# Optimization experiments

Hardware: AMD Instinct MI355X
Metric: run time of the kernel (lower is better)

## Reference

```python
import jax, jax.numpy as jnp
import numpy as np

N_EMBD = 1024
N_HEAD = 16
HEAD_DIM = N_EMBD // N_HEAD


def setup_inputs() -> dict:
    key = jax.random.key(0)
    kx, kq, kk, kv, ko = jax.random.split(key, 5)
    B, T = 4, 2048
    x = jax.random.normal(kx, (B, T, N_EMBD), dtype=jnp.float32)
    s = N_EMBD ** -0.5
    Wq = jax.random.normal(kq, (N_EMBD, N_EMBD), dtype=jnp.float32) * s
    Wk = jax.random.normal(kk, (N_EMBD, HEAD_DIM), dtype=jnp.float32) * s
    Wv = jax.random.normal(kv, (N_EMBD, HEAD_DIM), dtype=jnp.float32) * s
    Wo = jax.random.normal(ko, (N_EMBD, N_EMBD), dtype=jnp.float32) * s
    return {"x": x, "Wq": Wq, "Wk": Wk, "Wv": Wv, "Wo": Wo}


def reference(x, Wq, Wk, Wv, Wo):
    B, T, C = x.shape
    scale = HEAD_DIM ** -0.5
    # q: [B, H, T, D]; shared k, v: [B, T, D]
    q = (x @ Wq).reshape(B, T, N_HEAD, HEAD_DIM).transpose(0, 2, 1, 3)
    k = x @ Wk
    v = x @ Wv
    # scores: [B, H, T, T] (shared K head broadcast over H)
    att = jnp.einsum('bhtd,bsd->bhts', q, k) * scale
    causal = jnp.tril(jnp.ones((T, T), dtype=bool))
    att = jnp.where(causal, att, -jnp.inf)
    att = jax.nn.softmax(att, axis=-1)
    out = jnp.einsum('bhts,bsd->bhtd', att, v)  # [B, H, T, D]
    out = out.transpose(0, 2, 1, 3).reshape(B, T, C)
    return out @ Wo
```

## Files before the change

### kernel.cpp

```cpp
#include <hip/hip_runtime.h>

typedef __attribute__((ext_vector_type(8))) short short8;
typedef __attribute__((ext_vector_type(4))) float f32x4;

__device__ __forceinline__ unsigned short f2bf(float f) {
  unsigned u = __builtin_bit_cast(unsigned, f);
  u += 0x7fffu + ((u >> 16) & 1u);
  return (unsigned short)(u >> 16);
}
__device__ __forceinline__ unsigned pack_bf2_rtz(float p0, float p1) {
  return __builtin_amdgcn_perm(__builtin_bit_cast(unsigned, p1),
                               __builtin_bit_cast(unsigned, p0), 0x07060302u);
}

#define GLDS16(g, l)                                                          \
  __builtin_amdgcn_global_load_lds(                                           \
      (const __attribute__((address_space(1))) void*)(g),                     \
      (__attribute__((address_space(3))) void*)(l), 16, 0, 0)

#define QSCALE 0.18033688011112042f

__global__ void cast_x_bf16(const float4* __restrict__ in,
                            ushort4* __restrict__ out, int n4) {
  int i = blockIdx.x * blockDim.x + threadIdx.x;
  if (i >= n4) return;
  float4 v = in[i];
  ushort4 o;
  o.x = f2bf(v.x); o.y = f2bf(v.y); o.z = f2bf(v.z); o.w = f2bf(v.w);
  out[i] = o;
}

__global__ void transpose_cvt_all(const float* __restrict__ Wq,
                                  const float* __restrict__ Wk,
                                  const float* __restrict__ Wv,
                                  const float* __restrict__ Wo,
                                  unsigned short* __restrict__ Wcat,
                                  unsigned short* __restrict__ Wot) {
  __shared__ float tile[32][33];
  const int z = blockIdx.z;
  int bx = blockIdx.x;
  const float* in;
  unsigned short* out;
  int N;
  if (z == 0)      { in = Wq; out = Wcat;               N = 1024; }
  else if (z == 1) { in = Wo; out = Wot;                N = 1024; }
  else {
    if (bx < 2)      { in = Wk; out = Wcat + 1024 * 1024; N = 64; }
    else if (bx < 4) { in = Wv; out = Wcat + 1088 * 1024; N = 64; bx -= 2; }
    else return;
  }
  const int K = 1024;
  const int n0 = bx * 32, k0 = blockIdx.y * 32;
  const int tx = threadIdx.x, ty = threadIdx.y;
#pragma unroll
  for (int i = 0; i < 4; ++i)
    tile[ty + 8 * i][tx] = in[(size_t)(k0 + ty + 8 * i) * N + n0 + tx];
  __syncthreads();
#pragma unroll
  for (int i = 0; i < 4; ++i)
    out[(size_t)(n0 + ty + 8 * i) * K + k0 + tx] = f2bf(tile[tx][ty + 8 * i]);
}

__global__ void transpose_v(const unsigned short* __restrict__ Vr,
                            unsigned short* __restrict__ Vt) {
  __shared__ unsigned short tile[32][34];
  const int t0 = blockIdx.x * 32;
  const int d0 = blockIdx.y * 32;
  const int b = blockIdx.z;
  const int tx = threadIdx.x, ty = threadIdx.y;
#pragma unroll
  for (int i = 0; i < 4; ++i)
    tile[ty + 8 * i][tx] =
        Vr[(size_t)(b * 2048 + t0 + ty + 8 * i) * 64 + d0 + tx];
  __syncthreads();
#pragma unroll
  for (int i = 0; i < 4; ++i)
    Vt[((size_t)b * 64 + d0 + ty + 8 * i) * 2048 + t0 + tx] =
        tile[tx][ty + 8 * i];
}

template <int EPI>
__global__ __launch_bounds__(256) void gemm_bt(
    const unsigned short* __restrict__ A, const unsigned short* __restrict__ Bt,
    unsigned short* __restrict__ Cq, unsigned short* __restrict__ Ck,
    unsigned short* __restrict__ Cv, float* __restrict__ Cf, int N, int K) {
  __shared__ __align__(16) unsigned short As[128 * 64];
  __shared__ __align__(16) unsigned short Bs[128 * 64];
  const int tid = threadIdx.x;
  const int w = tid >> 6, lane = tid & 63;
  const int nwg = gridDim.x * gridDim.y;
  const int lid = blockIdx.y * gridDim.x + blockIdx.x;
  const int cpx = nwg >> 3;
  const int swz = (lid & 7) * cpx + (lid >> 3);
  const int m0 = (swz / gridDim.x) * 128, n0 = (swz % gridDim.x) * 128;
  const int wm = (w >> 1) * 64, wn = (w & 1) * 64;
  const int g = lane >> 4, c = lane & 15;
  const int lr = lane >> 3, lc = (lane & 7) * 8;

  f32x4 acc[4][4] = {};

  for (int k0 = 0; k0 < K; k0 += 64) {
#pragma unroll
    for (int i = 0; i < 4; ++i) {
      int ci = w * 4 + i;
      GLDS16(A + (size_t)(m0 + ci * 8 + lr) * K + k0 + lc, As + ci * 512);
      GLDS16(Bt + (size_t)(n0 + ci * 8 + lr) * K + k0 + lc, Bs + ci * 512);
    }
    __syncthreads();
#pragma unroll
    for (int kk = 0; kk < 2; ++kk) {
      const int col = kk * 32 + g * 8;
      short8 av[4], bv[4];
#pragma unroll
      for (int mi = 0; mi < 4; ++mi)
        av[mi] = *(const short8*)(As + (wm + mi * 16 + c) * 64 + col);
#pragma unroll
      for (int ni = 0; ni < 4; ++ni)
        bv[ni] = *(const short8*)(Bs + (wn + ni * 16 + c) * 64 + col);
#pragma unroll
      for (int mi = 0; mi < 4; ++mi)
#pragma unroll
        for (int ni = 0; ni < 4; ++ni)
          acc[mi][ni] = __builtin_amdgcn_mfma_f32_16x16x32_bf16(
              av[mi], bv[ni], acc[mi][ni], 0, 0, 0);
    }
    __syncthreads();
  }

#pragma unroll
  for (int mi = 0; mi < 4; ++mi) {
#pragma unroll
    for (int ni = 0; ni < 4; ++ni) {
      f32x4 a = acc[mi][ni];
      const int col = n0 + wn + ni * 16 + c;
#pragma unroll
      for (int r = 0; r < 4; ++r) {
        const int row = m0 + wm + mi * 16 + g * 4 + r;
        float v = a[r];
        if (EPI == 0) {
          if (col < 1024)
            Cq[(size_t)row * 1024 + col] = f2bf(v * QSCALE);
          else if (col < 1088)
            Ck[(size_t)row * 64 + (col - 1024)] = f2bf(v);
          else
            Cv[(size_t)row * 64 + (col - 1088)] = f2bf(v);
        } else {
          Cf[(size_t)row * N + col] = v;
        }
      }
    }
  }
}

__global__ __launch_bounds__(512, 4) void attn_mqa(
    const unsigned short* __restrict__ Q, const unsigned short* __restrict__ Kb,
    const unsigned short* __restrict__ Vt, unsigned short* __restrict__ Oc) {
  __shared__ __align__(16) unsigned short Kl[2][64 * 64];
  __shared__ __align__(16) unsigned short Vl[2][64 * 64];
  __shared__ __align__(16) unsigned short Pl[8][32 * 72];
  const int tid = threadIdx.x;
  const int w = tid >> 6, lane = tid & 63;
  const int bid = blockIdx.x;
  const int b = bid & 3;
  const int hp = (bid >> 2) & 7;
  const int qidx = (bid >> 5) & 7;
  const int half = (bid >> 8) & 1;
  const int qt = half ? (15 - qidx) : qidx;
  const int h = hp * 2 + (w >> 2);
  const int wq = w & 3;
  const int g = lane >> 4, c = lane & 15;
  const int swr = (c & 7) * 8;
  const int srow = tid >> 3;
  const int scs = ((tid & 7) ^ (srow & 7)) * 8;
  const unsigned short* Kbase = Kb + (size_t)b * 2048 * 64;
  const unsigned short* Vbase = Vt + (size_t)b * 64 * 2048;
  unsigned short* pw = Pl[w];
  unsigned* pd = (unsigned*)pw;

  short8 ones;
#pragma unroll
  for (int j = 0; j < 8; ++j) ones[j] = (short)0x3F80;

  const int qb = qt * 128 + wq * 32;

  short8 qf[2][2];
#pragma unroll
  for (int u = 0; u < 2; ++u)
#pragma unroll
    for (int kk = 0; kk < 2; ++kk)
      qf[u][kk] = *(const short8*)(Q + (size_t)(b * 2048 + qb + u * 16 + c) *
                                           1024 + h * 64 + kk * 32 + g * 8);

  f32x4 po[2][4] = {};
  f32x4 lac[2] = {};
  float m[2] = {-1e30f, -1e30f};

  GLDS16(Kbase + (size_t)srow * 64 + scs, &Kl[0][0] + tid * 8);
  GLDS16(Vbase + (size_t)srow * 2048 + scs, &Vl[0][0] + tid * 8);
  const unsigned short* kpf = Kbase + (size_t)(64 + srow) * 64 + scs;
  const unsigned short* vpf = Vbase + (size_t)srow * 2048 + 64 + scs;
  int cur = 0;
  const int nit = 2 * qt + 2;

  for (int it = 0; it < nit; ++it) {
    __syncthreads();

    if (it < nit - 1) {
      GLDS16(kpf, &Kl[cur ^ 1][0] + tid * 8);
      GLDS16(vpf, &Vl[cur ^ 1][0] + tid * 8);
      kpf += 64 * 64;
      vpf += 64;
    }

    const unsigned short* Kt = &Kl[cur][0];
    const unsigned short* Vc = &Vl[cur][0];
    const int kv0 = it * 64;

    f32x4 s[2][4] = {};
    __builtin_amdgcn_s_setprio(1);
#pragma unroll
    for (int kk = 0; kk < 2; ++kk) {
      const int col = (kk * 32 + g * 8) ^ swr;
#pragma unroll
      for (int f = 0; f < 4; ++f) {
        short8 kf = *(const short8*)(Kt + (f * 16 + c) * 64 + col);
        s[0][f] = __builtin_amdgcn_mfma_f32_16x16x32_bf16(kf, qf[0][kk],
                                                          s[0][f], 0, 0, 0);
        s[1][f] = __builtin_amdgcn_mfma_f32_16x16x32_bf16(kf, qf[1][kk],
                                                          s[1][f], 0, 0, 0);
      }
    }
    __builtin_amdgcn_s_setprio(0);

    float pm[2];
#pragma unroll
    for (int u = 0; u < 2; ++u) {
      if (kv0 + 63 > qb + u * 16) {
        const int qi = qb + u * 16 + c;
#pragma unroll
        for (int f = 0; f < 4; ++f)
#pragma unroll
          for (int r = 0; r < 4; ++r)
            if (kv0 + f * 16 + g * 4 + r > qi) s[u][f][r] = -1e30f;
      }
      const float t0 = fmaxf(fmaxf(s[u][0][0], s[u][0][1]), s[u][0][2]);
      const float t1 = fmaxf(fmaxf(s[u][0][3], s[u][1][0]), s[u][1][1]);
      const float t2 = fmaxf(fmaxf(s[u][1][2], s[u][1][3]), s[u][2][0]);
      const float t3 = fmaxf(fmaxf(s[u][2][1], s[u][2][2]), s[u][2][3]);
      const float t4 = fmaxf(fmaxf(s[u][3][0], s[u][3][1]), s[u][3][2]);
      const float u0 = fmaxf(fmaxf(t0, t1), t2);
      const float u1 = fmaxf(fmaxf(t3, t4), s[u][3][3]);
      pm[u] = fmaxf(u0, u1);
    }

    if (!__all(pm[0] <= m[0] + 8.0f && pm[1] <= m[1] + 8.0f)) {
#pragma unroll
      for (int u = 0; u < 2; ++u) {
        float pmu = fmaxf(pm[u], __shfl_xor(pm[u], 16, 64));
        pmu = fmaxf(pmu, __shfl_xor(pmu, 32, 64));
        const float mn = fmaxf(m[u], pmu);
        const float al = __builtin_amdgcn_exp2f(m[u] - mn);
        m[u] = mn;
#pragma unroll
        for (int r = 0; r < 4; ++r) {
          const float ar = __shfl(al, g * 4 + r, 64);
          lac[u][r] *= ar;
#pragma unroll
          for (int fd = 0; fd < 4; ++fd) po[u][fd][r] *= ar;
        }
      }
    }

#pragma unroll
    for (int u = 0; u < 2; ++u) {
#pragma unroll
      for (int f = 0; f < 4; ++f) {
        const float p0 = __builtin_amdgcn_exp2f(s[u][f][0] - m[u]);
        const float p1 = __builtin_amdgcn_exp2f(s[u][f][1] - m[u]);
        const float p2 = __builtin_amdgcn_exp2f(s[u][f][2] - m[u]);
        const float p3 = __builtin_amdgcn_exp2f(s[u][f][3] - m[u]);
        uint2 pk;
        pk.x = pack_bf2_rtz(p0, p1);
        pk.y = pack_bf2_rtz(p2, p3);
        *(uint2*)(pd + (u * 16 + c) * 36 + f * 8 + g * 2) = pk;
      }
    }

    __builtin_amdgcn_s_setprio(1);
#pragma unroll
    for (int kk = 0; kk < 2; ++kk) {
      short8 pa0 = *(const short8*)(pw + c * 72 + kk * 32 + g * 8);
      short8 pa1 = *(const short8*)(pw + (16 + c) * 72 + kk * 32 + g * 8);
      lac[0] = __builtin_amdgcn_mfma_f32_16x16x32_bf16(pa0, ones, lac[0], 0, 0, 0);
      lac[1] = __builtin_amdgcn_mfma_f32_16x16x32_bf16(pa1, ones, lac[1], 0, 0, 0);
      const int col = (kk * 32 + g * 8) ^ swr;
#pragma unroll
      for (int fd = 0; fd < 4; ++fd) {
        short8 vf = *(const short8*)(Vc + (fd * 16 + c) * 64 + col);
        po[0][fd] = __builtin_amdgcn_mfma_f32_16x16x32_bf16(pa0, vf, po[0][fd],
                                                            0, 0, 0);
        po[1][fd] = __builtin_amdgcn_mfma_f32_16x16x32_bf16(pa1, vf, po[1][fd],
                                                            0, 0, 0);
      }
    }
    __builtin_amdgcn_s_setprio(0);
    cur ^= 1;
  }

#pragma unroll
  for (int u = 0; u < 2; ++u) {
#pragma unroll
    for (int r = 0; r < 4; ++r) {
      const float inv = __builtin_amdgcn_rcpf(lac[u][r]);
      const int trow = qb + u * 16 + g * 4 + r;
#pragma unroll
      for (int fd = 0; fd < 4; ++fd)
        Oc[(size_t)(b * 2048 + trow) * 1024 + h * 64 + fd * 16 + c] =
            f2bf(po[u][fd][r] * inv);
    }
  }
}

extern "C" void kernel_launch(void* const* d_in, const int* in_sizes, int n_in,
                              void* d_out, int out_size, void* d_ws,
                              size_t ws_size, hipStream_t stream) {
  const float* x = (const float*)d_in[0];
  const float* Wq = (const float*)d_in[1];
  const float* Wk = (const float*)d_in[2];
  const float* Wv = (const float*)d_in[3];
  const float* Wo = (const float*)d_in[4];
  float* out = (float*)d_out;

  char* ws = (char*)d_ws;
  unsigned short* xb   = (unsigned short*)ws;
  unsigned short* Qb   = (unsigned short*)(ws + (size_t)(16u << 20));
  unsigned short* Attn = (unsigned short*)(ws + (size_t)(32u << 20));
  unsigned short* Wcat = (unsigned short*)(ws + (size_t)(48u << 20));
  unsigned short* Wot  = (unsigned short*)(ws + (size_t)(48u << 20) + 2359296);
  unsigned short* Kb   = (unsigned short*)(ws + (size_t)(48u << 20) + 2359296 + 2097152);
  unsigned short* Vtb  = (unsigned short*)(ws + (size_t)(48u << 20) + 2359296 + 2097152 + 1048576);
  unsigned short* Vrow = Attn;

  cast_x_bf16<<<8192, 256, 0, stream>>>((const float4*)x, (ushort4*)xb, 2097152);
  transpose_cvt_all<<<dim3(32, 32, 3), dim3(32, 8), 0, stream>>>(Wq, Wk, Wv, Wo,
                                                                 Wcat, Wot);

  gemm_bt<0><<<dim3(9, 64), 256, 0, stream>>>(xb, Wcat, Qb, Kb, Vrow, nullptr,
                                              1152, 1024);
  transpose_v<<<dim3(64, 2, 4), dim3(32, 8), 0, stream>>>(Vrow, Vtb);

  attn_mqa<<<512, 512, 0, stream>>>(Qb, Kb, Vtb, Attn);

  gemm_bt<1><<<dim3(8, 64), 256, 0, stream>>>(Attn, Wot, nullptr, nullptr,
                                              nullptr, out, 1024, 1024);
}
```

Baseline: 156.5 us.

## Split attention blocks to one head per 256-thread block with heavy-first ordering

The attention kernel now runs 1024 blocks of 256 threads, each handling a single head and a 128-row query tile, instead of 512 blocks of 512 threads covering two heads. Each thread issues two K and two V LDS prefetch loads per tile to fill the same 64x64 buffers. Query tiles are now scheduled longest-first (qt = 15 - qidx) instead of the previous paired ordering. The goal is finer-grained load balancing across the causal triangle and different occupancy, at the cost of K/V tiles being loaded from memory twice as often because they are no longer shared between two heads in one block.

```diff
diff --git a/kernel.cpp b/kernel.cpp
--- a/kernel.cpp
+++ b/kernel.cpp
@@ -152,26 +152,23 @@
   }
 }
 
-__global__ __launch_bounds__(512, 4) void attn_mqa(
+__global__ __launch_bounds__(256, 3) void attn_mqa(
     const unsigned short* __restrict__ Q, const unsigned short* __restrict__ Kb,
     const unsigned short* __restrict__ Vt, unsigned short* __restrict__ Oc) {
   __shared__ __align__(16) unsigned short Kl[2][64 * 64];
   __shared__ __align__(16) unsigned short Vl[2][64 * 64];
-  __shared__ __align__(16) unsigned short Pl[8][32 * 72];
+  __shared__ __align__(16) unsigned short Pl[4][32 * 72];
   const int tid = threadIdx.x;
   const int w = tid >> 6, lane = tid & 63;
   const int bid = blockIdx.x;
   const int b = bid & 3;
-  const int hp = (bid >> 2) & 7;
-  const int qidx = (bid >> 5) & 7;
-  const int half = (bid >> 8) & 1;
-  const int qt = half ? (15 - qidx) : qidx;
-  const int h = hp * 2 + (w >> 2);
-  const int wq = w & 3;
+  const int h = (bid >> 2) & 15;
+  const int qidx = (bid >> 6) & 15;
+  const int qt = 15 - qidx;
   const int g = lane >> 4, c = lane & 15;
   const int swr = (c & 7) * 8;
-  const int srow = tid >> 3;
-  const int scs = ((tid & 7) ^ (srow & 7)) * 8;
+  const int srow8 = tid >> 3;
+  const int scs = ((tid & 7) ^ (srow8 & 7)) * 8;
   const unsigned short* Kbase = Kb + (size_t)b * 2048 * 64;
   const unsigned short* Vbase = Vt + (size_t)b * 64 * 2048;
   unsigned short* pw = Pl[w];
@@ -181,7 +178,7 @@
 #pragma unroll
   for (int j = 0; j < 8; ++j) ones[j] = (short)0x3F80;
 
-  const int qb = qt * 128 + wq * 32;
+  const int qb = qt * 128 + w * 32;
 
   short8 qf[2][2];
 #pragma unroll
@@ -195,10 +192,14 @@
   f32x4 lac[2] = {};
   float m[2] = {-1e30f, -1e30f};
 
-  GLDS16(Kbase + (size_t)srow * 64 + scs, &Kl[0][0] + tid * 8);
-  GLDS16(Vbase + (size_t)srow * 2048 + scs, &Vl[0][0] + tid * 8);
-  const unsigned short* kpf = Kbase + (size_t)(64 + srow) * 64 + scs;
-  const unsigned short* vpf = Vbase + (size_t)srow * 2048 + 64 + scs;
+  const unsigned short* kpf = Kbase + (size_t)srow8 * 64 + scs;
+  const unsigned short* vpf = Vbase + (size_t)srow8 * 2048 + scs;
+  GLDS16(kpf, &Kl[0][0] + tid * 8);
+  GLDS16(kpf + 2048, &Kl[0][0] + tid * 8 + 2048);
+  GLDS16(vpf, &Vl[0][0] + tid * 8);
+  GLDS16(vpf + 65536, &Vl[0][0] + tid * 8 + 2048);
+  kpf += 4096;
+  vpf += 64;
   int cur = 0;
   const int nit = 2 * qt + 2;
 
@@ -206,9 +207,13 @@
     __syncthreads();
 
     if (it < nit - 1) {
-      GLDS16(kpf, &Kl[cur ^ 1][0] + tid * 8);
-      GLDS16(vpf, &Vl[cur ^ 1][0] + tid * 8);
-      kpf += 64 * 64;
+      unsigned short* kd = &Kl[cur ^ 1][0] + tid * 8;
+      unsigned short* vd = &Vl[cur ^ 1][0] + tid * 8;
+      GLDS16(kpf, kd);
+      GLDS16(kpf + 2048, kd + 2048);
+      GLDS16(vpf, vd);
+      GLDS16(vpf + 65536, vd + 2048);
+      kpf += 4096;
       vpf += 64;
     }
 
@@ -349,7 +354,7 @@
                                               1152, 1024);
   transpose_v<<<dim3(64, 2, 4), dim3(32, 8), 0, stream>>>(Vrow, Vtb);
 
-  attn_mqa<<<512, 512, 0, stream>>>(Qb, Kb, Vtb, Attn);
+  attn_mqa<<<1024, 256, 0, stream>>>(Qb, Kb, Vtb, Attn);
 
   gemm_bt<1><<<dim3(8, 64), 256, 0, stream>>>(Attn, Wot, nullptr, nullptr,
                                               nullptr, out, 1024, 1024);
```

New measurement: 146.9 us, median of 3. 6.1% less time.
